# Kernel optimization log

Measured on AMD Instinct MI355X. Metric: run time of the kernel, lower is better.

The kernel has to match this reference:

```python
import jax, jax.numpy as jnp
import numpy as np

BATCH = 8192
N_FEATURES = 512
DEPTH = 10
N_LEAVES = 2 ** DEPTH
ATOMS = N_FEATURES + 1  # include_one=True
TAU = 1.0


def eml(a, b):
    # Assumed definition of the custom binary eml op: smooth-max / log-sum-exp.
    # eml(a, b) = log(exp(a) + exp(b)), computed stably.
    return jnp.logaddexp(a, b)


def setup_inputs() -> dict:
    key = jax.random.key(0)
    k1, k2 = jax.random.split(key)
    X = jax.random.normal(k1, (BATCH, N_FEATURES), dtype=jnp.float32)
    leaf_logits = jax.random.normal(k2, (N_LEAVES, ATOMS), dtype=jnp.float32) * 0.1
    return {"X": X, "leaf_logits": leaf_logits}


def reference(X, leaf_logits):
    batch = X.shape[0]
    # atom values: prepend constant 1 (include_one=True) -> (batch, atoms)
    atom_values = jnp.concatenate([jnp.ones((batch, 1), dtype=X.dtype), X], axis=1)
    # softmax over atoms per leaf, then mix: (batch, n_leaves)
    weights = jax.nn.softmax(leaf_logits / TAU, axis=-1)
    current = jnp.einsum('ba,la->bl', atom_values, weights)
    # binary tree reduction: log2(n_leaves) steps over strided slices
    while current.shape[-1] > 1:
        current = eml(current[..., 0::2], current[..., 1::2])
    return current.squeeze(-1)  # (batch,)
```

## Files before the change

### kernel.cpp

```cpp
#include <hip/hip_runtime.h>
#include <hip/hip_bf16.h>

#define BATCH 8192
#define NF 512
#define NL 1024
#define ATOMS 513

typedef float float4v __attribute__((ext_vector_type(4)));
typedef int int4v __attribute__((ext_vector_type(4)));
typedef long long2v __attribute__((ext_vector_type(2)));

__device__ __forceinline__ unsigned char f2fp8(float x) {
    return (unsigned char)(__builtin_amdgcn_cvt_pk_fp8_f32(x, x, 0, false) & 0xff);
}

__device__ __forceinline__ void load_lds16(const void* g, void* ldsbase) {
    __builtin_amdgcn_global_load_lds(
        (const __attribute__((address_space(1))) unsigned int*)g,
        (__attribute__((address_space(3))) unsigned int*)ldsbase,
        16, 0, 0);
}


#define N_CONVERT_BLOCKS 512
#define N_SOFTMAX_BLOCKS 1024
#define N_ZERO_BLOCKS    33

__global__ void prep_kernel(const float* __restrict__ X,
                            const float* __restrict__ logits,
                            unsigned char* __restrict__ Xp,
                            unsigned char* __restrict__ Wp,
                            float* __restrict__ bias,
                            float* __restrict__ sumexp,
                            int* __restrict__ cnt) {
    int bi = blockIdx.x;
    int t  = threadIdx.x;

    if (bi < N_CONVERT_BLOCKS) {
        __shared__ unsigned char tile[16 * 512];
        int rt = bi;
        const float* base = X + (size_t)rt * 16 * 512;
#pragma unroll
        for (int i = 0; i < 8; ++i) {
            float4v v = *reinterpret_cast<const float4v*>(base + (size_t)i * 1024 + t * 4);
            int w = __builtin_amdgcn_cvt_pk_fp8_f32(v[0], v[1], 0, false);
            w = __builtin_amdgcn_cvt_pk_fp8_f32(v[2], v[3], w, true);
            reinterpret_cast<int*>(tile)[i * 256 + t] = w;
        }
        __syncthreads();
        int kp = t >> 5, j = t & 31;
#pragma unroll
        for (int e = 0; e < 2; ++e) {
            int ln = 2 * j + e;
            int l16 = ln & 15, quad = ln >> 4;
            const int* s0 = reinterpret_cast<const int*>(tile + l16 * 512 + (2 * kp) * 32 + quad * 8);
            const int* s1 = reinterpret_cast<const int*>(tile + l16 * 512 + (2 * kp + 1) * 32 + quad * 8);
            int4v o = (int4v){s0[0], s0[1], s1[0], s1[1]};
            *reinterpret_cast<int4v*>(Xp + (((size_t)rt * 8 + kp) * 64 + ln) * 16) = o;
        }
        return;
    }

    if (bi < N_CONVERT_BLOCKS + N_SOFTMAX_BLOCKS) {
        int l = bi - N_CONVERT_BLOCKS;
        int wave = t >> 6, lane = t & 63;
        const float* row = logits + (size_t)l * ATOMS;
        float v0 = row[t];
        float v1 = row[t + 256];
        float v2 = (t == 0) ? row[512] : -1e30f;

        __shared__ float red[8];
        float m = fmaxf(fmaxf(v0, v1), v2);
#pragma unroll
        for (int o = 32; o > 0; o >>= 1) m = fmaxf(m, __shfl_xor(m, o, 64));
        if (lane == 0) red[wave] = m;
        __syncthreads();
        float mx = fmaxf(fmaxf(red[0], red[1]), fmaxf(red[2], red[3]));

        float e0 = __expf(v0 - mx);
        float e1 = __expf(v1 - mx);
        float e2 = (t == 0) ? __expf(v2 - mx) : 0.f;
        float s = e0 + e1 + e2;
#pragma unroll
        for (int o = 32; o > 0; o >>= 1) s += __shfl_xor(s, o, 64);
        if (lane == 0) red[4 + wave] = s;
        __syncthreads();
        float inv = 1.f / (red[4] + red[5] + red[6] + red[7]);
        float inv512 = inv * 512.f;

        auto wp_off = [](int l_, int k_) -> size_t {
            int lt = l_ >> 4, l16_ = l_ & 15;
            int ks = k_ >> 5, kp_ = ks >> 1, half = ks & 1;
            int quad_ = (k_ >> 3) & 3, byt = k_ & 7;
            return ((size_t)((lt * 8 + kp_) * 64) + quad_ * 16 + l16_) * 16 + half * 8 + byt;
        };

        if (t == 0) {
            bias[l] = e0 * inv;
            Wp[wp_off(l, 511)] = f2fp8(e2 * inv512);
        } else {
            Wp[wp_off(l, t - 1)] = f2fp8(e0 * inv512);
        }
        Wp[wp_off(l, t + 255)] = f2fp8(e1 * inv512);
        return;
    }

    int i = (bi - N_CONVERT_BLOCKS - N_SOFTMAX_BLOCKS) * 256 + t;
    if (i < BATCH) sumexp[i] = 0.f;
    else { int j = i - BATCH; if (j < 64) cnt[j] = 0; }
}

__global__ __launch_bounds__(256, 2)
void gemm_lse_kernel(const unsigned char* __restrict__ Xp,
                     const unsigned char* __restrict__ Wp,
                     const float* __restrict__ bias,
                     float* __restrict__ sumexp,
                     int* __restrict__ cnt,
                     float* __restrict__ out) {
    __shared__ unsigned char Bl[64 * 1024];
    __shared__ float sums[128];
    __shared__ int lastFlag;

    int tid  = threadIdx.x;
    int wave = tid >> 6;
    int lane = tid & 63;
    int quad = lane >> 4;
    int l16  = lane & 15;

    int lg  = blockIdx.x & 7;
    int rsb = blockIdx.x >> 3;

    {
        const unsigned char* gb = Wp + (size_t)lg * 65536 + wave * 16384 + lane * 16;
        unsigned char* lb = Bl + wave * 16384;
#pragma unroll
        for (int j = 0; j < 16; ++j)
            load_lds16(gb + j * 1024, lb + j * 1024);
    }

    const unsigned char* pa = Xp + ((size_t)(rsb * 8 + wave * 2) * 8) * 1024 + lane * 16;

    float bl[8];
#pragma unroll
    for (int nt = 0; nt < 8; ++nt)
        bl[nt] = bias[lg * 128 + nt * 16 + l16];

    float4v acc[2][8];
#pragma unroll
    for (int mt = 0; mt < 2; ++mt)
#pragma unroll
        for (int nt = 0; nt < 8; ++nt)
            acc[mt][nt] = (float4v){0.f, 0.f, 0.f, 0.f};

    __syncthreads();

#pragma unroll
    for (int kp = 0; kp < 8; ++kp) {
        long2v af[2], bf[8];
#pragma unroll
        for (int mt = 0; mt < 2; ++mt)
            af[mt] = *reinterpret_cast<const long2v*>(pa + (size_t)mt * 8192 + kp * 1024);
#pragma unroll
        for (int nt = 0; nt < 8; ++nt)
            bf[nt] = *reinterpret_cast<const long2v*>(Bl + (nt * 8 + kp) * 1024 + lane * 16);

#pragma unroll
        for (int mt = 0; mt < 2; ++mt)
#pragma unroll
            for (int nt = 0; nt < 8; ++nt) {
                acc[mt][nt] = __builtin_amdgcn_mfma_f32_16x16x32_fp8_fp8(
                    af[mt][0], bf[nt][0], acc[mt][nt], 0, 0, 0);
                acc[mt][nt] = __builtin_amdgcn_mfma_f32_16x16x32_fp8_fp8(
                    af[mt][1], bf[nt][1], acc[mt][nt], 0, 0, 0);
            }
    }

    const float INV512 = 0.001953125f;
    float ps[2][4];
#pragma unroll
    for (int mt = 0; mt < 2; ++mt)
#pragma unroll
        for (int r = 0; r < 4; ++r) ps[mt][r] = 0.f;

#pragma unroll
    for (int nt = 0; nt < 8; ++nt)
#pragma unroll
        for (int mt = 0; mt < 2; ++mt)
#pragma unroll
            for (int r = 0; r < 4; ++r)
                ps[mt][r] += __expf(fmaf(acc[mt][nt][r], INV512, bl[nt]));

#pragma unroll
    for (int m = 1; m < 16; m <<= 1)
#pragma unroll
        for (int mt = 0; mt < 2; ++mt)
#pragma unroll
            for (int r = 0; r < 4; ++r)
                ps[mt][r] += __shfl_xor(ps[mt][r], m, 64);

    if (l16 == 0) {
#pragma unroll
        for (int mt = 0; mt < 2; ++mt)
#pragma unroll
            for (int r = 0; r < 4; ++r)
                sums[wave * 32 + mt * 16 + quad * 4 + r] = ps[mt][r];
    }
    __syncthreads();

    if (tid < 128)
        __hip_atomic_fetch_add(&sumexp[rsb * 128 + tid], sums[tid],
                               __ATOMIC_RELAXED, __HIP_MEMORY_SCOPE_AGENT);
    __syncthreads();

    if (tid == 0) {
        int old = __hip_atomic_fetch_add(&cnt[rsb], 1,
                                         __ATOMIC_RELAXED, __HIP_MEMORY_SCOPE_AGENT);
        lastFlag = (old == 7);
    }
    __syncthreads();

    if (lastFlag && tid < 128) {
        float s = __hip_atomic_fetch_add(&sumexp[rsb * 128 + tid], 0.0f,
                                         __ATOMIC_RELAXED, __HIP_MEMORY_SCOPE_AGENT);
        out[rsb * 128 + tid] = logf(s);
    }
}

extern "C" void kernel_launch(void* const* d_in, const int* in_sizes, int n_in,
                              void* d_out, int out_size, void* d_ws, size_t ws_size,
                              hipStream_t stream) {
    const float* X      = (const float*)d_in[0];
    const float* logits = (const float*)d_in[1];
    float* out = (float*)d_out;

    char* ws = (char*)d_ws;
    unsigned char* Xp = (unsigned char*)ws;
    unsigned char* Wp = (unsigned char*)(ws + (size_t)BATCH * NF);
    float* bias   = (float*)(ws + (size_t)BATCH * NF + (size_t)NL * NF);
    float* sumexp = (float*)((char*)bias + NL * sizeof(float));
    int*   cnt    = (int*)((char*)sumexp + BATCH * sizeof(float));

    prep_kernel<<<N_CONVERT_BLOCKS + N_SOFTMAX_BLOCKS + N_ZERO_BLOCKS, 256, 0, stream>>>(
        X, logits, Xp, Wp, bias, sumexp, cnt);
    gemm_lse_kernel<<<(BATCH / 128) * (NL / 128), 256, 0, stream>>>(
        Xp, Wp, bias, sumexp, cnt, out);
}
```

Baseline: 78.93 us.

## Hoist A-fragment loads, swap block order, use exp2 and direct atomics

Measured after the change: 76.44 us. 1.03x faster.

```diff
diff --git a/kernel.cpp b/kernel.cpp
--- a/kernel.cpp
+++ b/kernel.cpp
@@ -1,5 +1,6 @@
 #include <hip/hip_runtime.h>
 #include <hip/hip_bf16.h>
+#include <math.h>
 
 #define BATCH 8192
 #define NF 512
@@ -9,6 +10,8 @@
 typedef float float4v __attribute__((ext_vector_type(4)));
 typedef int int4v __attribute__((ext_vector_type(4)));
 typedef long long2v __attribute__((ext_vector_type(2)));
+
+#define LOG2E 1.44269504088896340736f
 
 __device__ __forceinline__ unsigned char f2fp8(float x) {
     return (unsigned char)(__builtin_amdgcn_cvt_pk_fp8_f32(x, x, 0, false) & 0xff);
@@ -96,7 +99,7 @@
         };
 
         if (t == 0) {
-            bias[l] = e0 * inv;
+            bias[l] = e0 * inv * LOG2E;
             Wp[wp_off(l, 511)] = f2fp8(e2 * inv512);
         } else {
             Wp[wp_off(l, t - 1)] = f2fp8(e0 * inv512);
@@ -118,7 +121,6 @@
                      int* __restrict__ cnt,
                      float* __restrict__ out) {
     __shared__ unsigned char Bl[64 * 1024];
-    __shared__ float sums[128];
     __shared__ int lastFlag;
 
     int tid  = threadIdx.x;
@@ -127,8 +129,8 @@
     int quad = lane >> 4;
     int l16  = lane & 15;
 
-    int lg  = blockIdx.x & 7;
-    int rsb = blockIdx.x >> 3;
+    int lg  = blockIdx.x >> 6;
+    int rsb = blockIdx.x & 63;
 
     {
         const unsigned char* gb = Wp + (size_t)lg * 65536 + wave * 16384 + lane * 16;
@@ -140,6 +142,13 @@
 
     const unsigned char* pa = Xp + ((size_t)(rsb * 8 + wave * 2) * 8) * 1024 + lane * 16;
 
+    long2v af[2][8];
+#pragma unroll
+    for (int mt = 0; mt < 2; ++mt)
+#pragma unroll
+        for (int kp = 0; kp < 8; ++kp)
+            af[mt][kp] = *reinterpret_cast<const long2v*>(pa + (size_t)mt * 8192 + kp * 1024);
+
     float bl[8];
 #pragma unroll
     for (int nt = 0; nt < 8; ++nt)
@@ -156,10 +165,7 @@
 
 #pragma unroll
     for (int kp = 0; kp < 8; ++kp) {
-        long2v af[2], bf[8];
-#pragma unroll
-        for (int mt = 0; mt < 2; ++mt)
-            af[mt] = *reinterpret_cast<const long2v*>(pa + (size_t)mt * 8192 + kp * 1024);
+        long2v bf[8];
 #pragma unroll
         for (int nt = 0; nt < 8; ++nt)
             bf[nt] = *reinterpret_cast<const long2v*>(Bl + (nt * 8 + kp) * 1024 + lane * 16);
@@ -169,13 +175,13 @@
 #pragma unroll
             for (int nt = 0; nt < 8; ++nt) {
                 acc[mt][nt] = __builtin_amdgcn_mfma_f32_16x16x32_fp8_fp8(
-                    af[mt][0], bf[nt][0], acc[mt][nt], 0, 0, 0);
+                    af[mt][kp][0], bf[nt][0], acc[mt][nt], 0, 0, 0);
                 acc[mt][nt] = __builtin_amdgcn_mfma_f32_16x16x32_fp8_fp8(
-                    af[mt][1], bf[nt][1], acc[mt][nt], 0, 0, 0);
+                    af[mt][kp][1], bf[nt][1], acc[mt][nt], 0, 0, 0);
             }
     }
 
-    const float INV512 = 0.001953125f;
+    const float C1 = 0.001953125f * LOG2E;
     float ps[2][4];
 #pragma unroll
     for (int mt = 0; mt < 2; ++mt)
@@ -188,7 +194,7 @@
         for (int mt = 0; mt < 2; ++mt)
 #pragma unroll
             for (int r = 0; r < 4; ++r)
-                ps[mt][r] += __expf(fmaf(acc[mt][nt][r], INV512, bl[nt]));
+                ps[mt][r] += exp2f(fmaf(acc[mt][nt][r], C1, bl[nt]));
 
 #pragma unroll
     for (int m = 1; m < 16; m <<= 1)
@@ -203,13 +209,10 @@
         for (int mt = 0; mt < 2; ++mt)
 #pragma unroll
             for (int r = 0; r < 4; ++r)
-                sums[wave * 32 + mt * 16 + quad * 4 + r] = ps[mt][r];
-    }
-    __syncthreads();
-
-    if (tid < 128)
-        __hip_atomic_fetch_add(&sumexp[rsb * 128 + tid], sums[tid],
-                               __ATOMIC_RELAXED, __HIP_MEMORY_SCOPE_AGENT);
+                __hip_atomic_fetch_add(&sumexp[rsb * 128 + wave * 32 + mt * 16 + quad * 4 + r],
+                                       ps[mt][r],
+                                       __ATOMIC_RELAXED, __HIP_MEMORY_SCOPE_AGENT);
+    }
     __syncthreads();
 
     if (tid == 0) {
```
